# Kernel tuning notes

Hardware: AMD Instinct MI355X
Metric: run time of the kernel (lower is better)

## Reference

```python
import jax, jax.numpy as jnp
import numpy as np

D_MODEL = 768
N_HEADS = 12
D_HEAD = D_MODEL // N_HEADS
TEMP = float(np.sqrt(D_HEAD))


def setup_inputs() -> dict:
    key = jax.random.key(0)
    ks = jax.random.split(key, 12)
    B, S, D = 8, 2048, D_MODEL
    patches = jax.random.normal(ks[0], (B, S, D), dtype=jnp.float32)
    in_weight = jax.random.uniform(ks[1], (D * 3, D), dtype=jnp.float32)
    in_bias = jax.random.uniform(ks[2], (D * 3,), dtype=jnp.float32)
    out_w = jax.random.normal(ks[3], (D, D), dtype=jnp.float32) * (1.0 / np.sqrt(D))
    out_b = jnp.zeros((D,), dtype=jnp.float32)
    mlp_w1 = jax.random.normal(ks[4], (4 * D, D), dtype=jnp.float32) * (1.0 / np.sqrt(D))
    mlp_b1 = jnp.zeros((4 * D,), dtype=jnp.float32)
    mlp_w2 = jax.random.normal(ks[5], (D, 4 * D), dtype=jnp.float32) * (1.0 / np.sqrt(4 * D))
    mlp_b2 = jnp.zeros((D,), dtype=jnp.float32)
    ln1_g = jnp.ones((D,), dtype=jnp.float32)
    ln1_b = jnp.zeros((D,), dtype=jnp.float32)
    ln2_g = jnp.ones((D,), dtype=jnp.float32)
    ln2_b = jnp.zeros((D,), dtype=jnp.float32)
    return {
        "patches": patches,
        "in_weight": in_weight, "in_bias": in_bias,
        "out_w": out_w, "out_b": out_b,
        "mlp_w1": mlp_w1, "mlp_b1": mlp_b1,
        "mlp_w2": mlp_w2, "mlp_b2": mlp_b2,
        "ln1_g": ln1_g, "ln1_b": ln1_b,
        "ln2_g": ln2_g, "ln2_b": ln2_b,
    }


def layer_norm(x, g, b, eps=1e-5):
    mu = jnp.mean(x, axis=-1, keepdims=True)
    var = jnp.var(x, axis=-1, keepdims=True)
    return (x - mu) * jax.lax.rsqrt(var + eps) * g + b


def mha(x, in_weight, in_bias, out_w, out_b):
    # Replicate quirky per-head reshape: [3D, D] -> [H, d_head, 3, D]
    W = in_weight.reshape(N_HEADS, D_HEAD, 3, D_MODEL)  # h, e, 3, d
    Bv = in_bias.reshape(N_HEADS, D_HEAD, 3)            # h, e, 3
    qw, kw, vw = W[:, :, 0, :], W[:, :, 1, :], W[:, :, 2, :]  # [H, e, D]
    qb, kb, vb = Bv[:, :, 0], Bv[:, :, 1], Bv[:, :, 2]        # [H, e]
    # Q,K,V per head: [B, H, S, e]
    Q = jnp.einsum('bsd,hed->bhse', x, qw) + qb[None, :, None, :]
    K = jnp.einsum('bsd,hed->bhse', x, kw) + kb[None, :, None, :]
    V = jnp.einsum('bsd,hed->bhse', x, vw) + vb[None, :, None, :]
    atn = jnp.einsum('bhse,bhte->bhst', Q, K)
    atn = jax.nn.softmax(atn / TEMP, axis=-1)
    # NOTE: original uses V (not atn @ V) as head output; heads concatenated over feature dim
    B_, H, S, e = V.shape
    heads = jnp.transpose(V, (0, 2, 1, 3)).reshape(B_, S, H * e)
    masks = jnp.sum(atn, axis=1)  # sum over heads: [B, S, S]
    out = heads @ out_w.T + out_b
    return out, masks


def reference(patches, in_weight, in_bias, out_w, out_b,
              mlp_w1, mlp_b1, mlp_w2, mlp_b2,
              ln1_g, ln1_b, ln2_g, ln2_b):
    x = layer_norm(patches, ln1_g, ln1_b)
    sa, _ = mha(x, in_weight, in_bias, out_w, out_b)
    x = sa + x  # dropout = identity (eval)
    x = layer_norm(x, ln2_g, ln2_b)
    h = jax.nn.selu(x @ mlp_w1.T + mlp_b1)
    x = (h @ mlp_w2.T + mlp_b2) + x
    return x
```

## Files before the change

kernel.cpp:

```cpp
#include <hip/hip_runtime.h>


typedef __bf16 bf16;
typedef __bf16 bf16x8 __attribute__((ext_vector_type(8)));
typedef __bf16 bf16x4 __attribute__((ext_vector_type(4)));
typedef float  f32x4  __attribute__((ext_vector_type(4)));

#define N_ROWS  16384

__global__ __launch_bounds__(256) void cast_kernel(const float* __restrict__ x,
                                                   bf16* __restrict__ y, int n4) {
  int i = blockIdx.x * 256 + threadIdx.x;
  if (i >= n4) return;
  float4 v = ((const float4*)x)[i];
  bf16x4 o = {(bf16)v.x, (bf16)v.y, (bf16)v.z, (bf16)v.w};
  *(bf16x4*)(y + 4 * (size_t)i) = o;
}

__global__ __launch_bounds__(256) void wvt_kernel(const float* __restrict__ in_weight,
                                                  bf16* __restrict__ wvt) {
  int k = blockIdx.x * 256 + threadIdx.x;
  int j = blockIdx.y;
  wvt[(size_t)k * 768 + j] = (bf16)in_weight[((size_t)j * 3 + 2) * 768 + k];
}

__global__ __launch_bounds__(64) void bias_combine_kernel(const float* __restrict__ out_w,
                                                          const float* __restrict__ in_bias,
                                                          const float* __restrict__ out_b,
                                                          float* __restrict__ bc) {
  int n = blockIdx.x, l = threadIdx.x;
  float s = 0.f;
  for (int j = l; j < 768; j += 64) s += out_w[(size_t)n * 768 + j] * in_bias[j * 3 + 2];
#pragma unroll
  for (int off = 32; off > 0; off >>= 1) s += __shfl_xor(s, off, 64);
  if (l == 0) bc[n] = s + out_b[n];
}

__global__ __launch_bounds__(256) void ln_kernel(const float* __restrict__ x,
                                                 const float* __restrict__ g,
                                                 const float* __restrict__ b,
                                                 bf16* __restrict__ y) {
  const int row = blockIdx.x;
  const float* xr = x + (size_t)row * 768;
  float v[3], s1 = 0.f, s2 = 0.f;
#pragma unroll
  for (int i = 0; i < 3; ++i) {
    v[i] = xr[threadIdx.x + i * 256];
    s1 += v[i];
    s2 += v[i] * v[i];
  }
#pragma unroll
  for (int off = 32; off > 0; off >>= 1) {
    s1 += __shfl_xor(s1, off, 64);
    s2 += __shfl_xor(s2, off, 64);
  }
  __shared__ float red[8];
  int w = threadIdx.x >> 6, l = threadIdx.x & 63;
  if (l == 0) { red[w * 2] = s1; red[w * 2 + 1] = s2; }
  __syncthreads();
  s1 = red[0] + red[2] + red[4] + red[6];
  s2 = red[1] + red[3] + red[5] + red[7];
  const float mu = s1 * (1.f / 768.f);
  const float var = s2 * (1.f / 768.f) - mu * mu;
  const float rstd = rsqrtf(var + 1e-5f);
#pragma unroll
  for (int i = 0; i < 3; ++i) {
    int d = threadIdx.x + i * 256;
    y[(size_t)row * 768 + d] = (bf16)((v[i] - mu) * rstd * g[d] + b[d]);
  }
}

template <int EPI>
__global__ __launch_bounds__(256) void gemm_bt(const bf16* __restrict__ A,
                                               const bf16* __restrict__ B,
                                               const float* __restrict__ bias,
                                               const bf16* __restrict__ resid,
                                               void* __restrict__ out,
                                               int M, int N, int K) {
  __shared__ bf16 sA[128 * 32];
  __shared__ bf16 sB[128 * 32];
  const int tid = threadIdx.x;
  const int w = tid >> 6, l = tid & 63;
  const int wr = w >> 1, wc = w & 1;
  const int q = l >> 4, m16 = l & 15;

  int mtile, ntile;
  {
    const int L = blockIdx.y * gridDim.x + blockIdx.x;
    const int gy = gridDim.y;
    if ((gy & 7) == 0) {
      const int mpx = gy >> 3;
      const int xcd = L & 7;
      const int slot = L >> 3;
      mtile = xcd * mpx + (slot % mpx);
      ntile = slot / mpx;
    } else {
      mtile = blockIdx.y; ntile = blockIdx.x;
    }
  }
  const long tileM = (long)mtile * 128;
  const long tileN = (long)ntile * 128;

  f32x4 acc[4][4] = {};

  for (int k0 = 0; k0 < K; k0 += 32) {
#pragma unroll
    for (int i = 0; i < 2; ++i) {
      const int ch = tid + i * 256;
      const int row = ch >> 2;
      const int clog = ((ch & 3) - (row >> 1)) & 3;
      const bf16* ga = A + (tileM + row) * (long)K + k0 + clog * 8;
      const bf16* gb = B + (tileN + row) * (long)K + k0 + clog * 8;
      __builtin_amdgcn_global_load_lds(
          (const __attribute__((address_space(1))) void*)ga,
          (__attribute__((address_space(3))) void*)(&sA[ch * 8]), 16, 0, 0);
      __builtin_amdgcn_global_load_lds(
          (const __attribute__((address_space(1))) void*)gb,
          (__attribute__((address_space(3))) void*)(&sB[ch * 8]), 16, 0, 0);
    }
    __syncthreads();

    bf16x8 af[4], bfr[4];
#pragma unroll
    for (int mi = 0; mi < 4; ++mi) {
      const int r = wr * 64 + mi * 16 + m16;
      af[mi] = *(const bf16x8*)&sA[r * 32 + (((q + (r >> 1)) & 3) << 3)];
    }
#pragma unroll
    for (int ni = 0; ni < 4; ++ni) {
      const int r = wc * 64 + ni * 16 + m16;
      bfr[ni] = *(const bf16x8*)&sB[r * 32 + (((q + (r >> 1)) & 3) << 3)];
    }
#pragma unroll
    for (int mi = 0; mi < 4; ++mi)
#pragma unroll
      for (int ni = 0; ni < 4; ++ni)
        acc[mi][ni] = __builtin_amdgcn_mfma_f32_16x16x32_bf16(af[mi], bfr[ni],
                                                              acc[mi][ni], 0, 0, 0);
    __syncthreads();
  }

  const long colBase = tileN + wc * 64 + m16;
  const long rowBase = tileM + wr * 64 + q * 4;
#pragma unroll
  for (int mi = 0; mi < 4; ++mi) {
#pragma unroll
    for (int r = 0; r < 4; ++r) {
      const long row = rowBase + mi * 16 + r;
#pragma unroll
      for (int ni = 0; ni < 4; ++ni) {
        const long col = colBase + ni * 16;
        float v = acc[mi][ni][r];
        if (EPI == 0) {
          ((bf16*)out)[row * N + col] = (bf16)v;
        } else if (EPI == 1) {
          v += bias[col] + (float)resid[row * N + col];
          ((float*)out)[row * N + col] = v;
        } else {
          v += bias[col];
          v = v > 0.f ? 1.0507009873554805f * v
                      : 1.0507009873554805f * 1.6732632423543772f * (__expf(v) - 1.f);
          ((bf16*)out)[row * N + col] = (bf16)v;
        }
      }
    }
  }
}

extern "C" void kernel_launch(void* const* d_in, const int* in_sizes, int n_in,
                              void* d_out, int out_size, void* d_ws, size_t ws_size,
                              hipStream_t stream) {
  const float* patches   = (const float*)d_in[0];
  const float* in_weight = (const float*)d_in[1];
  const float* in_bias   = (const float*)d_in[2];
  const float* out_w     = (const float*)d_in[3];
  const float* out_b     = (const float*)d_in[4];
  const float* mlp_w1    = (const float*)d_in[5];
  const float* mlp_b1    = (const float*)d_in[6];
  const float* mlp_w2    = (const float*)d_in[7];
  const float* mlp_b2    = (const float*)d_in[8];
  const float* ln1_g     = (const float*)d_in[9];
  const float* ln1_b     = (const float*)d_in[10];
  const float* ln2_g     = (const float*)d_in[11];
  const float* ln2_b     = (const float*)d_in[12];

  char* ws = (char*)d_ws;
  const size_t MB = 1024 * 1024;
  bf16* Wc   = (bf16*)(ws + 0);
  bf16* w1b  = (bf16*)(ws + 2 * MB);
  bf16* w2b  = (bf16*)(ws + 8 * MB);
  bf16* owb  = (bf16*)(ws + 14 * MB);
  bf16* wvt  = (bf16*)(ws + 16 * MB);
  float* bc  = (float*)(ws + 18 * MB);
  bf16* X1   = (bf16*)(ws + 20 * MB);
  bf16* X3   = (bf16*)(ws + 20 * MB);
  bf16* H    = (bf16*)(ws + 48 * MB);
  float* X2  = (float*)d_out;

  cast_kernel<<<(3072 * 768 / 4 + 255) / 256, 256, 0, stream>>>(mlp_w1, w1b, 3072 * 768 / 4);
  cast_kernel<<<(768 * 3072 / 4 + 255) / 256, 256, 0, stream>>>(mlp_w2, w2b, 768 * 3072 / 4);
  cast_kernel<<<(768 * 768 / 4 + 255) / 256, 256, 0, stream>>>(out_w, owb, 768 * 768 / 4);
  wvt_kernel<<<dim3(3, 768), 256, 0, stream>>>(in_weight, wvt);
  bias_combine_kernel<<<768, 64, 0, stream>>>(out_w, in_bias, out_b, bc);
  gemm_bt<0><<<dim3(6, 6), 256, 0, stream>>>(owb, wvt, nullptr, nullptr, Wc, 768, 768, 768);

  ln_kernel<<<N_ROWS, 256, 0, stream>>>(patches, ln1_g, ln1_b, X1);
  gemm_bt<1><<<dim3(6, 128), 256, 0, stream>>>(X1, Wc, bc, X1, X2, N_ROWS, 768, 768);
  ln_kernel<<<N_ROWS, 256, 0, stream>>>(X2, ln2_g, ln2_b, X3);
  gemm_bt<2><<<dim3(24, 128), 256, 0, stream>>>(X3, w1b, mlp_b1, nullptr, H, N_ROWS, 3072, 768);
  gemm_bt<1><<<dim3(6, 128), 256, 0, stream>>>(H, w2b, mlp_b2, X3, d_out, N_ROWS, 768, 3072);
}
```

Before: 476.2 us.

## Double-buffer LDS tiles in bf16 GEMM to overlap global loads with MFMA

Converts the GEMM main loop to ping-pong shared-memory buffers. The next K-slice is issued via global_load_lds before the current slice's MFMAs run, leaving one barrier per iteration instead of two. Address and swizzle offsets are also hoisted out of the loop. Shared memory use doubles to 32KB per block, which may reduce occupancy, and the overlap depends on the compiler not inserting a full vmcnt wait before the LDS reads.

```diff
diff --git a/kernel.cpp b/kernel.cpp
--- a/kernel.cpp
+++ b/kernel.cpp
@@ -7,6 +7,9 @@
 typedef float  f32x4  __attribute__((ext_vector_type(4)));
 
 #define N_ROWS  16384
+
+#define AS1(p) ((const __attribute__((address_space(1))) void*)(p))
+#define AS3(p) ((__attribute__((address_space(3))) void*)(p))
 
 __global__ __launch_bounds__(256) void cast_kernel(const float* __restrict__ x,
                                                    bf16* __restrict__ y, int n4) {
@@ -77,8 +80,8 @@
                                                const bf16* __restrict__ resid,
                                                void* __restrict__ out,
                                                int M, int N, int K) {
-  __shared__ bf16 sA[128 * 32];
-  __shared__ bf16 sB[128 * 32];
+  __shared__ bf16 sA0[128 * 32], sA1[128 * 32];
+  __shared__ bf16 sB0[128 * 32], sB1[128 * 32];
   const int tid = threadIdx.x;
   const int w = tid >> 6, l = tid & 63;
   const int wr = w >> 1, wc = w & 1;
@@ -101,43 +104,76 @@
   const long tileM = (long)mtile * 128;
   const long tileN = (long)ntile * 128;
 
+  const int ch0 = tid, ch1 = tid + 256;
+  const int row0 = ch0 >> 2, row1 = ch1 >> 2;
+  const int cl0 = ((ch0 & 3) - (row0 >> 1)) & 3;
+  const int cl1 = ((ch1 & 3) - (row1 >> 1)) & 3;
+  const bf16* ga0 = A + (tileM + row0) * (long)K + cl0 * 8;
+  const bf16* ga1 = A + (tileM + row1) * (long)K + cl1 * 8;
+  const bf16* gb0 = B + (tileN + row0) * (long)K + cl0 * 8;
+  const bf16* gb1 = B + (tileN + row1) * (long)K + cl1 * 8;
+  const int ld0 = ch0 * 8, ld1 = ch1 * 8;
+
+  int offA[4], offB[4];
+#pragma unroll
+  for (int mi = 0; mi < 4; ++mi) {
+    const int r = wr * 64 + mi * 16 + m16;
+    offA[mi] = r * 32 + (((q + (r >> 1)) & 3) << 3);
+  }
+#pragma unroll
+  for (int ni = 0; ni < 4; ++ni) {
+    const int r = wc * 64 + ni * 16 + m16;
+    offB[ni] = r * 32 + (((q + (r >> 1)) & 3) << 3);
+  }
+
   f32x4 acc[4][4] = {};
 
-  for (int k0 = 0; k0 < K; k0 += 32) {
-#pragma unroll
-    for (int i = 0; i < 2; ++i) {
-      const int ch = tid + i * 256;
-      const int row = ch >> 2;
-      const int clog = ((ch & 3) - (row >> 1)) & 3;
-      const bf16* ga = A + (tileM + row) * (long)K + k0 + clog * 8;
-      const bf16* gb = B + (tileN + row) * (long)K + k0 + clog * 8;
-      __builtin_amdgcn_global_load_lds(
-          (const __attribute__((address_space(1))) void*)ga,
-          (__attribute__((address_space(3))) void*)(&sA[ch * 8]), 16, 0, 0);
-      __builtin_amdgcn_global_load_lds(
-          (const __attribute__((address_space(1))) void*)gb,
-          (__attribute__((address_space(3))) void*)(&sB[ch * 8]), 16, 0, 0);
-    }
-    __syncthreads();
+  __builtin_amdgcn_global_load_lds(AS1(ga0), AS3(&sA0[ld0]), 16, 0, 0);
+  __builtin_amdgcn_global_load_lds(AS1(ga1), AS3(&sA0[ld1]), 16, 0, 0);
+  __builtin_amdgcn_global_load_lds(AS1(gb0), AS3(&sB0[ld0]), 16, 0, 0);
+  __builtin_amdgcn_global_load_lds(AS1(gb1), AS3(&sB0[ld1]), 16, 0, 0);
+  __syncthreads();
+
+  const bf16 *cra = sA0, *crb = sB0;
+  bf16 *nxa = sA1, *nxb = sB1;
+
+#pragma unroll 2
+  for (long k0 = 32; k0 < K; k0 += 32) {
+    __builtin_amdgcn_global_load_lds(AS1(ga0 + k0), AS3(&nxa[ld0]), 16, 0, 0);
+    __builtin_amdgcn_global_load_lds(AS1(ga1 + k0), AS3(&nxa[ld1]), 16, 0, 0);
+    __builtin_amdgcn_global_load_lds(AS1(gb0 + k0), AS3(&nxb[ld0]), 16, 0, 0);
+    __builtin_amdgcn_global_load_lds(AS1(gb1 + k0), AS3(&nxb[ld1]), 16, 0, 0);
 
     bf16x8 af[4], bfr[4];
 #pragma unroll
-    for (int mi = 0; mi < 4; ++mi) {
-      const int r = wr * 64 + mi * 16 + m16;
-      af[mi] = *(const bf16x8*)&sA[r * 32 + (((q + (r >> 1)) & 3) << 3)];
-    }
-#pragma unroll
-    for (int ni = 0; ni < 4; ++ni) {
-      const int r = wc * 64 + ni * 16 + m16;
-      bfr[ni] = *(const bf16x8*)&sB[r * 32 + (((q + (r >> 1)) & 3) << 3)];
-    }
+    for (int mi = 0; mi < 4; ++mi) af[mi] = *(const bf16x8*)&cra[offA[mi]];
+#pragma unroll
+    for (int ni = 0; ni < 4; ++ni) bfr[ni] = *(const bf16x8*)&crb[offB[ni]];
 #pragma unroll
     for (int mi = 0; mi < 4; ++mi)
 #pragma unroll
       for (int ni = 0; ni < 4; ++ni)
         acc[mi][ni] = __builtin_amdgcn_mfma_f32_16x16x32_bf16(af[mi], bfr[ni],
                                                               acc[mi][ni], 0, 0, 0);
+
     __syncthreads();
+
+    const bf16* ta = cra; cra = nxa; nxa = (bf16*)ta;
+    const bf16* tb = crb; crb = nxb; nxb = (bf16*)tb;
+  }
+
+  {
+    bf16x8 af[4], bfr[4];
+#pragma unroll
+    for (int mi = 0; mi < 4; ++mi) af[mi] = *(const bf16x8*)&cra[offA[mi]];
+#pragma unroll
+    for (int ni = 0; ni < 4; ++ni) bfr[ni] = *(const bf16x8*)&crb[offB[ni]];
+#pragma unroll
+    for (int mi = 0; mi < 4; ++mi)
+#pragma unroll
+      for (int ni = 0; ni < 4; ++ni)
+        acc[mi][ni] = __builtin_amdgcn_mfma_f32_16x16x32_bf16(af[mi], bfr[ni],
+                                                              acc[mi][ni], 0, 0, 0);
   }
 
   const long colBase = tileN + wc * 64 + m16;
```

Result: faster. 426.8 us (-10.4%).
